# Kernel tuning notes

Hardware: AMD Instinct MI355X
Metric: run time of the kernel (lower is better)

Reference implementation:

```python
import jax, jax.numpy as jnp
import numpy as np

N_CHEM = 200000
N_DIS = 200000
D = 256
L = 2  # num_layers
R = 4  # relations: 0=cause(chem->dis),1=relate(chem->dis),2=rev_relate(dis->chem),3=child(dis->dis)
E = 500000


def setup_inputs() -> dict:
    key = jax.random.key(0)
    ks = jax.random.split(key, 12)
    x_chem = jax.random.normal(ks[0], (N_CHEM, D), dtype=jnp.float32)
    x_dis = jax.random.normal(ks[1], (N_DIS, D), dtype=jnp.float32)
    ei_cause = jax.random.randint(ks[2], (2, E), 0, N_CHEM, dtype=jnp.int32)
    ei_relate = jax.random.randint(ks[3], (2, E), 0, N_CHEM, dtype=jnp.int32)
    ei_rev = jax.random.randint(ks[4], (2, E), 0, N_DIS, dtype=jnp.int32)
    ei_child = jax.random.randint(ks[5], (2, E), 0, N_DIS, dtype=jnp.int32)
    scale = 1.0 / np.sqrt(D)
    # PyG SAGEConv params per (layer, relation): lin_l (W+b, applied to mean-aggregated
    # neighbors) and lin_r (W only, applied to destination/root features).
    Wl = jax.random.normal(ks[6], (L, R, D, D), dtype=jnp.float32) * scale
    bl = jnp.zeros((L, R, D), dtype=jnp.float32)
    Wr = jax.random.normal(ks[7], (L, R, D, D), dtype=jnp.float32) * scale
    return {"x_chem": x_chem, "x_dis": x_dis, "Wl": Wl, "bl": bl, "Wr": Wr,
            "ei_cause": ei_cause, "ei_relate": ei_relate, "ei_rev": ei_rev,
            "ei_child": ei_child}


def _sage(x_src, x_dst, ei, Wl, bl, Wr, n_dst):
    # SAGEConv: lin_l(mean_{j in N(i)} x_j) + lin_r(x_i)
    src, dst = ei[0], ei[1]
    msg = jnp.take(x_src, src, axis=0)                      # [E, D] gather
    s = jax.ops.segment_sum(msg, dst, num_segments=n_dst)   # [n_dst, D]
    cnt = jax.ops.segment_sum(jnp.ones((ei.shape[1],), x_src.dtype), dst,
                              num_segments=n_dst)
    mean = s / jnp.maximum(cnt, 1.0)[:, None]               # zero-degree -> 0
    return mean @ Wl + bl + x_dst @ Wr


def _hetero_layer(x_chem, x_dis, Wl, bl, Wr, ei_cause, ei_relate, ei_rev, ei_child):
    # HeteroConv(aggr='sum'): sum conv outputs per destination node type.
    out_dis = (_sage(x_chem, x_dis, ei_cause, Wl[0], bl[0], Wr[0], N_DIS)
               + _sage(x_chem, x_dis, ei_relate, Wl[1], bl[1], Wr[1], N_DIS)
               + _sage(x_dis, x_dis, ei_child, Wl[3], bl[3], Wr[3], N_DIS))
    out_chem = _sage(x_dis, x_chem, ei_rev, Wl[2], bl[2], Wr[2], N_CHEM)
    return out_chem, out_dis


def reference(x_chem, x_dis, Wl, bl, Wr, ei_cause, ei_relate, ei_rev, ei_child):
    # layers[:-1]: conv -> relu -> dropout(p=0, identity)
    for l in range(L - 1):
        x_chem, x_dis = _hetero_layer(x_chem, x_dis, Wl[l], bl[l], Wr[l],
                                      ei_cause, ei_relate, ei_rev, ei_child)
        x_chem = jax.nn.relu(x_chem)
        x_dis = jax.nn.relu(x_dis)
    # last layer: conv only
    x_chem, x_dis = _hetero_layer(x_chem, x_dis, Wl[L - 1], bl[L - 1], Wr[L - 1],
                                  ei_cause, ei_relate, ei_rev, ei_child)
    return x_chem, x_dis
```

## Files before the change

### kernel.cpp

```cpp
#include <hip/hip_runtime.h>

#define D_FEAT 256
constexpr int N_CHEM = 200000;
constexpr int N_DIS  = 200000;
constexpr int N_EDGE = 500000;
constexpr int NROWS  = 200000;
constexpr int NPAD   = 200064;
constexpr int NCNT   = 4 * NROWS;
constexpr int NEALL  = 4 * N_EDGE;

constexpr int PB_CNT = (NEALL + 255) / 256;
constexpr int PB_CVT = NROWS * D_FEAT / 4 / 256;
constexpr int PB_WT  = 1538;

typedef _Float16 f16x8 __attribute__((ext_vector_type(8)));
typedef _Float16 f16x4 __attribute__((ext_vector_type(4)));
typedef float    f32x4 __attribute__((ext_vector_type(4)));

__device__ __forceinline__ void gload_lds16(const void* g, void* l) {
    __builtin_amdgcn_global_load_lds(
        (const __attribute__((address_space(1))) void*)g,
        (__attribute__((address_space(3))) void*)l, 16, 0, 0);
}

__global__ __launch_bounds__(256) void prep_k(
    const int* __restrict__ e0, const int* __restrict__ e1,
    const int* __restrict__ e2, const int* __restrict__ e3,
    int* __restrict__ cnt,
    const float* __restrict__ x_chem, _Float16* __restrict__ xb_chem,
    const float* __restrict__ x_dis,  _Float16* __restrict__ xb_dis,
    const float* __restrict__ Wl, const float* __restrict__ Wr,
    const float* __restrict__ bl,
    _Float16* __restrict__ WT_dis, _Float16* __restrict__ WT_chem,
    float* __restrict__ bsum) {
    const int b = blockIdx.x;
    if (b < PB_CNT) {
        const int g = b * 256 + threadIdx.x;
        if (g >= NEALL) return;
        const int r = g / N_EDGE;
        const int le = g - r * N_EDGE;
        const int* e = (r == 0) ? e0 : (r == 1) ? e1 : (r == 2) ? e2 : e3;
        atomicAdd(&cnt[r * NROWS + e[N_EDGE + le]], 1);
    } else if (b < PB_CNT + 2 * PB_CVT) {
        const int b1 = b - PB_CNT;
        const float* in = (b1 < PB_CVT) ? x_chem : x_dis;
        _Float16* out = (b1 < PB_CVT) ? xb_chem : xb_dis;
        const int i = (b1 % PB_CVT) * 256 + threadIdx.x;
        const float4 v = reinterpret_cast<const float4*>(in)[i];
        f16x4 o;
        o[0] = (_Float16)v.x; o[1] = (_Float16)v.y;
        o[2] = (_Float16)v.z; o[3] = (_Float16)v.w;
        reinterpret_cast<f16x4*>(out)[i] = o;
    } else {
        const int b2 = b - PB_CNT - 2 * PB_CVT;
        const int l = b2 / PB_WT;
        const int idx = (b2 % PB_WT) * 256 + threadIdx.x;
        const float* Wl_l = Wl + (size_t)l * 4 * 65536;
        const float* Wr_l = Wr + (size_t)l * 4 * 65536;
        if (idx < 262144) {
            const int n = idx >> 10, k = idx & 1023, seg = k >> 8, kk = k & 255;
            float v;
            if (seg == 0)
                v = Wr_l[kk * 256 + n] + Wr_l[65536 + kk * 256 + n] + Wr_l[3 * 65536 + kk * 256 + n];
            else if (seg == 1) v = Wl_l[kk * 256 + n];
            else if (seg == 2) v = Wl_l[65536 + kk * 256 + n];
            else               v = Wl_l[3 * 65536 + kk * 256 + n];
            WT_dis[(size_t)l * 262144 + idx] = (_Float16)v;
        } else if (idx < 393216) {
            const int li = idx - 262144;
            const int n = li >> 9, k = li & 511, seg = k >> 8, kk = k & 255;
            const float v = (seg == 0) ? Wr_l[2 * 65536 + kk * 256 + n]
                                       : Wl_l[2 * 65536 + kk * 256 + n];
            WT_chem[(size_t)l * 131072 + li] = (_Float16)v;
        } else if (idx < 393216 + 256) {
            const int n = idx - 393216;
            const float* bb = bl + (size_t)l * 1024;
            bsum[l * 256 + n] = bb[n] + bb[256 + n] + bb[3 * 256 + n];
        }
    }
}

__global__ __launch_bounds__(256) void scan1_k(const int* __restrict__ cnt,
                                               int* __restrict__ offs,
                                               int* __restrict__ cursor,
                                               int* __restrict__ bsums, int n) {
    __shared__ int s[256];
    const int t = threadIdx.x;
    const int i = blockIdx.x * 256 + t;
    const int v = (i < n) ? cnt[i] : 0;
    s[t] = v;
    __syncthreads();
#pragma unroll
    for (int d = 1; d < 256; d <<= 1) {
        const int x = (t >= d) ? s[t - d] : 0;
        __syncthreads();
        s[t] += x;
        __syncthreads();
    }
    if (i < n) {
        const int o = s[t] - v;
        offs[i] = o;
        cursor[i] = o;
    }
    if (t == 255) bsums[blockIdx.x] = s[255];
}

__global__ __launch_bounds__(1024) void scan2_k(int* __restrict__ bsums, int nb) {
    __shared__ int s[1024];
    const int t = threadIdx.x;
    int v[4];
    int sum = 0;
#pragma unroll
    for (int q = 0; q < 4; ++q) {
        const int i = t * 4 + q;
        v[q] = (i < nb) ? bsums[i] : 0;
        sum += v[q];
    }
    s[t] = sum;
    __syncthreads();
#pragma unroll
    for (int d = 1; d < 1024; d <<= 1) {
        const int x = (t >= d) ? s[t - d] : 0;
        __syncthreads();
        s[t] += x;
        __syncthreads();
    }
    int base = s[t] - sum;
#pragma unroll
    for (int q = 0; q < 4; ++q) {
        const int i = t * 4 + q;
        if (i < nb) {
            const int tmp = v[q];
            bsums[i] = base;
            base += tmp;
        }
    }
}

__global__ __launch_bounds__(256) void fill_all_k(
    const int* __restrict__ e0, const int* __restrict__ e1,
    const int* __restrict__ e2, const int* __restrict__ e3,
    int* __restrict__ cursor, const int* __restrict__ bsums,
    int* __restrict__ csr) {
    const int g = blockIdx.x * 256 + threadIdx.x;
    if (g >= NEALL) return;
    const int r = g / N_EDGE;
    const int le = g - r * N_EDGE;
    const int* e = (r == 0) ? e0 : (r == 1) ? e1 : (r == 2) ? e2 : e3;
    const int d = r * NROWS + e[N_EDGE + le];
    const int p = atomicAdd(&cursor[d], 1) + bsums[d >> 8];
    csr[p] = e[le];
}

__global__ __launch_bounds__(256) void gather_all_k(
    const _Float16* __restrict__ srcA, const _Float16* __restrict__ srcB,
    const int* __restrict__ csr, const int* __restrict__ offs,
    const int* __restrict__ bsums, const int* __restrict__ cnt,
    _Float16* __restrict__ chunkbuf, int crp, int base, int rows) {
    const int y = blockIdx.y;
    const int rel = (y == 0) ? 0 : (y == 1) ? 1 : (y == 2) ? 3 : 2;
    const _Float16* x = (y < 2) ? srcA : srcB;
    _Float16* agg = chunkbuf + (size_t)y * crp * D_FEAT;

    const int wid = threadIdx.x >> 6;
    const int lane = threadIdx.x & 63;
    const int grp = lane >> 4;
    const int li  = lane & 15;
    const int lrow = blockIdx.x * 16 + wid * 4 + grp;
    if (lrow >= rows) return;
    const int g = rel * NROWS + base + lrow;
    const int start = offs[g] + bsums[g >> 8];
    const int n = cnt[g];
    float a0[8] = {0,0,0,0,0,0,0,0}, a1[8] = {0,0,0,0,0,0,0,0};
    const _Float16* xb = x + li * 16;
    for (int j = 0; j < n; j += 4) {
        const int rem = n - j;
        const int i0 = start + j;
        const int c1 = (rem > 1) ? 1 : 0;
        const int c2 = (rem > 2) ? 2 : 0;
        const int c3 = (rem > 3) ? 3 : 0;
        const int s0 = csr[i0];
        const int s1 = csr[i0 + c1];
        const int s2 = csr[i0 + c2];
        const int s3 = csr[i0 + c3];
        const float w1 = c1 ? 1.f : 0.f;
        const float w2 = c2 ? 1.f : 0.f;
        const float w3 = c3 ? 1.f : 0.f;
        const f16x8 u0a = *reinterpret_cast<const f16x8*>(xb + (size_t)s0 * D_FEAT);
        const f16x8 u0b = *reinterpret_cast<const f16x8*>(xb + (size_t)s0 * D_FEAT + 8);
        const f16x8 u1a = *reinterpret_cast<const f16x8*>(xb + (size_t)s1 * D_FEAT);
        const f16x8 u1b = *reinterpret_cast<const f16x8*>(xb + (size_t)s1 * D_FEAT + 8);
        const f16x8 u2a = *reinterpret_cast<const f16x8*>(xb + (size_t)s2 * D_FEAT);
        const f16x8 u2b = *reinterpret_cast<const f16x8*>(xb + (size_t)s2 * D_FEAT + 8);
        const f16x8 u3a = *reinterpret_cast<const f16x8*>(xb + (size_t)s3 * D_FEAT);
        const f16x8 u3b = *reinterpret_cast<const f16x8*>(xb + (size_t)s3 * D_FEAT + 8);
#pragma unroll
        for (int q = 0; q < 8; ++q) {
            a0[q] += (float)u0a[q];
            a0[q] = fmaf(w1, (float)u1a[q], a0[q]);
            a0[q] = fmaf(w2, (float)u2a[q], a0[q]);
            a0[q] = fmaf(w3, (float)u3a[q], a0[q]);
            a1[q] += (float)u0b[q];
            a1[q] = fmaf(w1, (float)u1b[q], a1[q]);
            a1[q] = fmaf(w2, (float)u2b[q], a1[q]);
            a1[q] = fmaf(w3, (float)u3b[q], a1[q]);
        }
    }
    const float inv = 1.0f / fmaxf((float)n, 1.0f);
    f16x8 o0, o1;
#pragma unroll
    for (int q = 0; q < 8; ++q) {
        o0[q] = (_Float16)(a0[q] * inv);
        o1[q] = (_Float16)(a1[q] * inv);
    }
    _Float16* ap = agg + (size_t)lrow * D_FEAT + li * 16;
    *reinterpret_cast<f16x8*>(ap) = o0;
    *reinterpret_cast<f16x8*>(ap + 8) = o1;
}

template <int NSEG, bool RELU_OUT>
__device__ __forceinline__ void gemm_body(
    _Float16* __restrict__ Asl, _Float16* __restrict__ Bsl,
    const _Float16* __restrict__ A0, const _Float16* __restrict__ A1,
    const _Float16* __restrict__ A2, const _Float16* __restrict__ A3,
    const _Float16* __restrict__ WT, const float* __restrict__ bias,
    float* __restrict__ Cf, _Float16* __restrict__ Ch, int vrows, int row0) {
    constexpr int KT = NSEG * 256;
    constexpr int NS = KT / 64;
    const int t = threadIdx.x;
    const int w = t >> 6, l = t & 63;
    const int wm = w >> 2, wn = w & 3;
    const int fr = l & 15, ko = (l >> 4) << 3;

    f32x4 acc[4][4];
#pragma unroll
    for (int m = 0; m < 4; ++m)
#pragma unroll
        for (int n = 0; n < 4; ++n) acc[m][n] = f32x4{0.f, 0.f, 0.f, 0.f};

    const int srow = t >> 3;
    const int schk = t & 7;
    const int gchk = schk ^ (srow & 7);
    const int rsw  = (fr & 7) << 3;

    auto STAGE = [&](int buf, int ks) {
        const int seg = ks >> 2;
        const _Float16* Ab = (seg == 0) ? A0 : ((seg == 1) ? A1 : ((seg == 2) ? A2 : A3));
        const int kofs = ((ks & 3) << 6) + gchk * 8;
        _Float16* asl = Asl + buf * 8192;
        _Float16* bsl = Bsl + buf * 16384;
#pragma unroll
        for (int is = 0; is < 2; ++is)
            gload_lds16(Ab + (size_t)(row0 + is * 64 + srow) * D_FEAT + kofs,
                        asl + is * 4096 + w * 512);
#pragma unroll
        for (int is = 0; is < 4; ++is)
            gload_lds16(WT + (size_t)(is * 64 + srow) * KT + seg * 256 + kofs,
                        bsl + is * 4096 + w * 512);
    };

    auto COMPUTE = [&](int buf) {
        const _Float16* asl = Asl + buf * 8192;
        const _Float16* bsl = Bsl + buf * 16384;
#pragma unroll
        for (int kk = 0; kk < 64; kk += 32) {
            f16x8 af[4], bf[4];
            const int ksw = (kk + ko) ^ rsw;
#pragma unroll
            for (int m = 0; m < 4; ++m)
                af[m] = *reinterpret_cast<const f16x8*>(&asl[(wm * 64 + m * 16 + fr) * 64 + ksw]);
#pragma unroll
            for (int n = 0; n < 4; ++n)
                bf[n] = *reinterpret_cast<const f16x8*>(&bsl[(wn * 64 + n * 16 + fr) * 64 + ksw]);
#pragma unroll
            for (int m = 0; m < 4; ++m)
#pragma unroll
                for (int n = 0; n < 4; ++n)
                    acc[m][n] = __builtin_amdgcn_mfma_f32_16x16x32_f16(af[m], bf[n], acc[m][n], 0, 0, 0);
        }
    };

    STAGE(0, 0);
    int cur = 0;
    for (int ks = 0; ks < NS - 1; ++ks) {
        STAGE(cur ^ 1, ks + 1);
        asm volatile("s_waitcnt vmcnt(6)" ::: "memory");
        __builtin_amdgcn_s_barrier();
        __builtin_amdgcn_sched_barrier(0);
        COMPUTE(cur);
        __builtin_amdgcn_sched_barrier(0);
        __builtin_amdgcn_s_barrier();
        __builtin_amdgcn_sched_barrier(0);
        cur ^= 1;
    }
    asm volatile("s_waitcnt vmcnt(0)" ::: "memory");
    __builtin_amdgcn_s_barrier();
    __builtin_amdgcn_sched_barrier(0);
    COMPUTE(cur);

    const int cro = (l >> 4) << 2;
#pragma unroll
    for (int n = 0; n < 4; ++n) {
        const int col = wn * 64 + n * 16 + fr;
        const float bi = bias[col];
#pragma unroll
        for (int m = 0; m < 4; ++m) {
            const int rbase = row0 + wm * 64 + m * 16 + cro;
#pragma unroll
            for (int j = 0; j < 4; ++j) {
                const int r = rbase + j;
                if (r < vrows) {
                    const float v = acc[m][n][j] + bi;
                    if constexpr (RELU_OUT)
                        Ch[(size_t)r * D_FEAT + col] = (_Float16)fmaxf(v, 0.f);
                    else
                        Cf[(size_t)r * D_FEAT + col] = v;
                }
            }
        }
    }
}

template <bool RELU_OUT>
__global__ __launch_bounds__(512) void gemm2_k(
    const _Float16* __restrict__ A0d, const _Float16* __restrict__ A1,
    const _Float16* __restrict__ A2, const _Float16* __restrict__ A3,
    const _Float16* __restrict__ WTd, const float* __restrict__ biasd,
    float* __restrict__ Cfd, _Float16* __restrict__ Chd,
    const _Float16* __restrict__ A0c, const _Float16* __restrict__ A4,
    const _Float16* __restrict__ WTc, const float* __restrict__ biasc,
    float* __restrict__ Cfc, _Float16* __restrict__ Chc, int vrows) {
    __shared__ _Float16 Asl[2 * 128 * 64];
    __shared__ _Float16 Bsl[2 * 256 * 64];
    const int row0 = blockIdx.x * 128;
    if (blockIdx.y == 0)
        gemm_body<4, RELU_OUT>(Asl, Bsl, A0d, A1, A2, A3, WTd, biasd, Cfd, Chd, vrows, row0);
    else
        gemm_body<2, RELU_OUT>(Asl, Bsl, A0c, A4, nullptr, nullptr, WTc, biasc, Cfc, Chc, vrows, row0);
}

extern "C" void kernel_launch(void* const* d_in, const int* in_sizes, int n_in,
                              void* d_out, int out_size, void* d_ws, size_t ws_size,
                              hipStream_t stream) {
    const float* x_chem = (const float*)d_in[0];
    const float* x_dis  = (const float*)d_in[1];
    const float* Wl     = (const float*)d_in[2];
    const float* bl     = (const float*)d_in[3];
    const float* Wr     = (const float*)d_in[4];
    const int* ei[4] = {(const int*)d_in[5],
                        (const int*)d_in[6],
                        (const int*)d_in[7],
                        (const int*)d_in[8]};

    float* out_chem = (float*)d_out;
    float* out_dis  = out_chem + (size_t)N_CHEM * D_FEAT;

    constexpr size_t FB = (size_t)NPAD * D_FEAT * 2;
    char* w = (char*)d_ws;
    _Float16* h_chem  = (_Float16*)(w);
    _Float16* h_dis   = (_Float16*)(w + FB);
    _Float16* xb_chem = (_Float16*)(w + 2 * FB);
    _Float16* xb_dis  = (_Float16*)(w + 3 * FB);
    char* p = w + 4 * FB;
    int* csr    = (int*)(p);              p += 8000000;
    int* counts = (int*)(p);              p += 3200000;
    int* offs   = (int*)(p);              p += 3200000;
    int* cursor = (int*)(p);              p += 3200000;
    int* bsums  = (int*)(p);              p += 16384;
    _Float16* WT_dis  = (_Float16*)(p);   p += 1048576;
    _Float16* WT_chem = (_Float16*)(p);   p += 524288;
    float* bsum = (float*)(p);            p += 2048;
    _Float16* chunkbuf = (_Float16*)(p);

    const size_t FIXED = (size_t)(p - w);
    long long avail = (long long)ws_size - (long long)FIXED;
    int crp = 51200;
    if (avail < (long long)crp * 2048) {
        long long c = avail / 2048;
        if (c > NPAD) c = NPAD;
        crp = (int)(c & ~127LL);
        if (crp < 128) crp = 128;
    }
    const int nc = (NROWS + crp - 1) / crp;

    const int eall_grid = (NEALL + 255) / 256;
    const int scan_blocks = (NCNT + 255) / 256;
    hipMemsetAsync(counts, 0, NCNT * sizeof(int), stream);
    prep_k<<<PB_CNT + 2 * PB_CVT + 2 * PB_WT, 256, 0, stream>>>(
        ei[0], ei[1], ei[2], ei[3], counts,
        x_chem, xb_chem, x_dis, xb_dis, Wl, Wr, bl, WT_dis, WT_chem, bsum);
    scan1_k<<<scan_blocks, 256, 0, stream>>>(counts, offs, cursor, bsums, NCNT);
    scan2_k<<<1, 1024, 0, stream>>>(bsums, scan_blocks);
    fill_all_k<<<eall_grid, 256, 0, stream>>>(ei[0], ei[1], ei[2], ei[3], cursor, bsums, csr);

    _Float16* slot0 = chunkbuf;
    _Float16* slot1 = chunkbuf + (size_t)1 * crp * D_FEAT;
    _Float16* slot2 = chunkbuf + (size_t)2 * crp * D_FEAT;
    _Float16* slot3 = chunkbuf + (size_t)3 * crp * D_FEAT;

    for (int layer = 0; layer < 2; ++layer) {
        const _Float16* srcA = layer ? h_chem : xb_chem;
        const _Float16* srcB = layer ? h_dis  : xb_dis;
        const _Float16* WTd = WT_dis + (size_t)layer * 262144;
        const _Float16* WTc = WT_chem + (size_t)layer * 131072;
        const float* biasd = bsum + layer * 256;
        const float* biasc = bl + (layer * 4 + 2) * 256;

        for (int i = 0; i < nc; ++i) {
            const int base = i * crp;
            const int rows = (NROWS - base < crp) ? (NROWS - base) : crp;
            const int rows_pad = (rows + 127) & ~127;
            const size_t boff = (size_t)base * D_FEAT;
            const dim3 ggrid((rows + 15) / 16, 4);
            const dim3 mgrid(rows_pad / 128, 2);
            gather_all_k<<<ggrid, 256, 0, stream>>>(srcA, srcB, csr, offs, bsums,
                                                    counts, chunkbuf, crp, base, rows);
            if (layer == 0)
                gemm2_k<true><<<mgrid, 512, 0, stream>>>(
                    srcB + boff, slot0, slot1, slot2, WTd, biasd,
                    nullptr, h_dis + boff,
                    srcA + boff, slot3, WTc, biasc,
                    nullptr, h_chem + boff, rows);
            else
                gemm2_k<false><<<mgrid, 512, 0, stream>>>(
                    srcB + boff, slot0, slot1, slot2, WTd, biasd,
                    out_dis + boff, nullptr,
                    srcA + boff, slot3, WTc, biasc,
                    out_chem + boff, nullptr, rows);
        }
    }
}
```

Before: 1.659 ms.

## Split GEMM into 128x128 tiles with 256-thread blocks and XCD-aware block remap

Changes the fused dis/chem GEMM from a 128x256 output tile with 512 threads to a 128x128 tile with 256 threads. The grid becomes one-dimensional, and block indices are remapped so that consecutive logical tiles, which share A rows, land on the same XCD for L2 reuse. Smaller tiles halve LDS usage and allow more resident blocks, but the A operand is now loaded twice, once per column half.

```diff
diff --git a/kernel.cpp b/kernel.cpp
--- a/kernel.cpp
+++ b/kernel.cpp
@@ -220,16 +220,17 @@
 
 template <int NSEG, bool RELU_OUT>
 __device__ __forceinline__ void gemm_body(
-    _Float16* __restrict__ Asl, _Float16* __restrict__ Bsl,
+    _Float16* __restrict__ AslBase, _Float16* __restrict__ BslBase,
     const _Float16* __restrict__ A0, const _Float16* __restrict__ A1,
     const _Float16* __restrict__ A2, const _Float16* __restrict__ A3,
     const _Float16* __restrict__ WT, const float* __restrict__ bias,
-    float* __restrict__ Cf, _Float16* __restrict__ Ch, int vrows, int row0) {
+    float* __restrict__ Cf, _Float16* __restrict__ Ch, int vrows,
+    int row0, int col0) {
     constexpr int KT = NSEG * 256;
     constexpr int NS = KT / 64;
     const int t = threadIdx.x;
     const int w = t >> 6, l = t & 63;
-    const int wm = w >> 2, wn = w & 3;
+    const int wm = w & 1, wn = w >> 1;
     const int fr = l & 15, ko = (l >> 4) << 3;
 
     f32x4 acc[4][4];
@@ -247,21 +248,20 @@
         const int seg = ks >> 2;
         const _Float16* Ab = (seg == 0) ? A0 : ((seg == 1) ? A1 : ((seg == 2) ? A2 : A3));
         const int kofs = ((ks & 3) << 6) + gchk * 8;
-        _Float16* asl = Asl + buf * 8192;
-        _Float16* bsl = Bsl + buf * 16384;
-#pragma unroll
-        for (int is = 0; is < 2; ++is)
-            gload_lds16(Ab + (size_t)(row0 + is * 64 + srow) * D_FEAT + kofs,
-                        asl + is * 4096 + w * 512);
-#pragma unroll
-        for (int is = 0; is < 4; ++is)
-            gload_lds16(WT + (size_t)(is * 64 + srow) * KT + seg * 256 + kofs,
-                        bsl + is * 4096 + w * 512);
+        _Float16* asl = AslBase + buf * 8192;
+        _Float16* bsl = BslBase + buf * 8192;
+#pragma unroll
+        for (int is = 0; is < 4; ++is) {
+            gload_lds16(Ab + (size_t)(row0 + is * 32 + srow) * D_FEAT + kofs,
+                        asl + is * 2048 + w * 512);
+            gload_lds16(WT + (size_t)(col0 + is * 32 + srow) * KT + seg * 256 + kofs,
+                        bsl + is * 2048 + w * 512);
+        }
     };
 
     auto COMPUTE = [&](int buf) {
-        const _Float16* asl = Asl + buf * 8192;
-        const _Float16* bsl = Bsl + buf * 16384;
+        const _Float16* asl = AslBase + buf * 8192;
+        const _Float16* bsl = BslBase + buf * 8192;
 #pragma unroll
         for (int kk = 0; kk < 64; kk += 32) {
             f16x8 af[4], bf[4];
@@ -284,7 +284,7 @@
     int cur = 0;
     for (int ks = 0; ks < NS - 1; ++ks) {
         STAGE(cur ^ 1, ks + 1);
-        asm volatile("s_waitcnt vmcnt(6)" ::: "memory");
+        asm volatile("s_waitcnt vmcnt(8)" ::: "memory");
         __builtin_amdgcn_s_barrier();
         __builtin_amdgcn_sched_barrier(0);
         COMPUTE(cur);
@@ -301,7 +301,7 @@
     const int cro = (l >> 4) << 2;
 #pragma unroll
     for (int n = 0; n < 4; ++n) {
-        const int col = wn * 64 + n * 16 + fr;
+        const int col = col0 + wn * 64 + n * 16 + fr;
         const float bi = bias[col];
 #pragma unroll
         for (int m = 0; m < 4; ++m) {
@@ -322,21 +322,26 @@
 }
 
 template <bool RELU_OUT>
-__global__ __launch_bounds__(512) void gemm2_k(
+__global__ __launch_bounds__(256) void gemm2_k(
     const _Float16* __restrict__ A0d, const _Float16* __restrict__ A1,
     const _Float16* __restrict__ A2, const _Float16* __restrict__ A3,
     const _Float16* __restrict__ WTd, const float* __restrict__ biasd,
     float* __restrict__ Cfd, _Float16* __restrict__ Chd,
     const _Float16* __restrict__ A0c, const _Float16* __restrict__ A4,
     const _Float16* __restrict__ WTc, const float* __restrict__ biasc,
-    float* __restrict__ Cfc, _Float16* __restrict__ Chc, int vrows) {
+    float* __restrict__ Cfc, _Float16* __restrict__ Chc, int vrows, int T) {
     __shared__ _Float16 Asl[2 * 128 * 64];
-    __shared__ _Float16 Bsl[2 * 256 * 64];
-    const int row0 = blockIdx.x * 128;
-    if (blockIdx.y == 0)
-        gemm_body<4, RELU_OUT>(Asl, Bsl, A0d, A1, A2, A3, WTd, biasd, Cfd, Chd, vrows, row0);
+    __shared__ _Float16 Bsl[2 * 128 * 64];
+    const int b = blockIdx.x;
+    const int xcd = b & 7, loc = b >> 3;
+    const int q = T >> 3, r = T & 7;
+    const int u = ((xcd < r) ? xcd * (q + 1) : r * (q + 1) + (xcd - r) * q) + loc;
+    const int x = u >> 2, y = (u >> 1) & 1, z = u & 1;
+    const int row0 = x * 128, col0 = y * 128;
+    if (z == 0)
+        gemm_body<4, RELU_OUT>(Asl, Bsl, A0d, A1, A2, A3, WTd, biasd, Cfd, Chd, vrows, row0, col0);
     else
-        gemm_body<2, RELU_OUT>(Asl, Bsl, A0c, A4, nullptr, nullptr, WTc, biasc, Cfc, Chc, vrows, row0);
+        gemm_body<2, RELU_OUT>(Asl, Bsl, A0c, A4, nullptr, nullptr, WTc, biasc, Cfc, Chc, vrows, row0, col0);
 }
 
 extern "C" void kernel_launch(void* const* d_in, const int* in_sizes, int n_in,
@@ -412,21 +417,21 @@
             const int rows_pad = (rows + 127) & ~127;
             const size_t boff = (size_t)base * D_FEAT;
             const dim3 ggrid((rows + 15) / 16, 4);
-            const dim3 mgrid(rows_pad / 128, 2);
+            const int T = (rows_pad / 128) * 4;
             gather_all_k<<<ggrid, 256, 0, stream>>>(srcA, srcB, csr, offs, bsums,
                                                     counts, chunkbuf, crp, base, rows);
             if (layer == 0)
-                gemm2_k<true><<<mgrid, 512, 0, stream>>>(
+                gemm2_k<true><<<T, 256, 0, stream>>>(
                     srcB + boff, slot0, slot1, slot2, WTd, biasd,
                     nullptr, h_dis + boff,
                     srcA + boff, slot3, WTc, biasc,
-                    nullptr, h_chem + boff, rows);
+                    nullptr, h_chem + boff, rows, T);
             else
-                gemm2_k<false><<<mgrid, 512, 0, stream>>>(
+                gemm2_k<false><<<T, 256, 0, stream>>>(
                     srcB + boff, slot0, slot1, slot2, WTd, biasd,
                     out_dis + boff, nullptr,
                     srcA + boff, slot3, WTc, biasc,
-                    out_chem + boff, nullptr, rows);
-        }
-    }
-}
+                    out_chem + boff, nullptr, rows, T);
+        }
+    }
+}
```

Result: slower. 1.743 ms, median of 4 (+5.1%).
